# Kernel tuning notes

Hardware: AMD Instinct MI355X
Metric: run time of the kernel (lower is better)

The kernel has to match this reference:

```python
import jax, jax.numpy as jnp
import numpy as np

N_UNITS = 512
H = 8
D_K = N_UNITS // H  # 64
B = 4
T = 1024


def setup_inputs() -> dict:
    key = jax.random.key(0)
    ks = jax.random.split(key, 10)
    s = 0.02
    return {
        "x": jax.random.normal(ks[0], (B * T, N_UNITS), dtype=jnp.float32),
        "pos_k": jax.random.normal(ks[1], (T, T, D_K), dtype=jnp.float32),
        "batch_size": B,
        "Wq": jax.random.normal(ks[2], (N_UNITS, N_UNITS), dtype=jnp.float32) * s,
        "bq": jax.random.normal(ks[3], (N_UNITS,), dtype=jnp.float32) * s,
        "Wk": jax.random.normal(ks[4], (N_UNITS, N_UNITS), dtype=jnp.float32) * s,
        "bk": jax.random.normal(ks[5], (N_UNITS,), dtype=jnp.float32) * s,
        "Wv": jax.random.normal(ks[6], (N_UNITS, N_UNITS), dtype=jnp.float32) * s,
        "bv": jax.random.normal(ks[7], (N_UNITS,), dtype=jnp.float32) * s,
        "Wo": jax.random.normal(ks[8], (N_UNITS, N_UNITS), dtype=jnp.float32) * s,
        "bo": jax.random.normal(ks[9], (N_UNITS,), dtype=jnp.float32) * s,
    }


def reference(x, pos_k, batch_size, Wq, bq, Wk, bk, Wv, bv, Wo, bo):
    # x: [B*T, n_units]; pos_k: [T, T, d_k]
    q = (x @ Wq + bq).reshape(batch_size, -1, H, D_K).transpose(0, 2, 1, 3)  # [B,h,T,d]
    k = (x @ Wk + bk).reshape(batch_size, -1, H, D_K).transpose(0, 2, 1, 3)
    v = (x @ Wv + bv).reshape(batch_size, -1, H, D_K).transpose(0, 2, 1, 3)
    att_score = jnp.einsum("bhqd,bhkd->bhqk", q, k)
    # relative-position score: per query position t, q[:,:,t] @ pos_k[t].T
    att_score_pos = jnp.einsum("bhqd,qkd->bhqk", q, pos_k)
    scores = (att_score + att_score_pos) / np.sqrt(D_K).astype(np.float32)
    att = jax.nn.softmax(scores, axis=3)  # dropout p=0 -> identity (eval)
    out = jnp.einsum("bhqk,bhkd->bhqd", att, v)  # [B,h,T,d]
    out = out.transpose(0, 2, 1, 3).reshape(-1, H * D_K)  # [B*T, n_units]
    return out @ Wo + bo
```

## Files before the change

### kernel.cpp

```cpp
#include <hip/hip_runtime.h>


#define TT 1024
#define DH 64
#define NH 8
#define NBH 32
#define NU 512
#define NROW 4096

typedef __bf16 bf16;
typedef bf16 bf16x8 __attribute__((ext_vector_type(8)));
typedef bf16 bf16x4 __attribute__((ext_vector_type(4)));
typedef float f32x4 __attribute__((ext_vector_type(4)));

#define MFMA16(a, b, c) __builtin_amdgcn_mfma_f32_16x16x32_bf16(a, b, c, 0, 0, 0)

__global__ __launch_bounds__(256) void cvtx_k(const float* __restrict__ x,
                                              bf16* __restrict__ xb) {
  int i = blockIdx.x * 256 + threadIdx.x;
  float4 v = ((const float4*)x)[i];
  bf16x4 o = {(bf16)v.x, (bf16)v.y, (bf16)v.z, (bf16)v.w};
  ((bf16x4*)xb)[i] = o;
}

__global__ __launch_bounds__(256) void wtrans_k(const float* __restrict__ Wq,
                                                const float* __restrict__ Wk,
                                                const float* __restrict__ Wv,
                                                const float* __restrict__ Wo,
                                                bf16* __restrict__ wt) {
  int n = blockIdx.x * 256 + threadIdx.x;
  int k0 = blockIdx.y * 64;
  int w = blockIdx.z;
  const float* W = (w == 0) ? Wq : (w == 1) ? Wk : (w == 2) ? Wv : Wo;
  bf16* o = wt + ((size_t)w * NU + n) * NU;
  for (int kk = 0; kk < 64; kk += 8) {
    bf16x8 v;
#pragma unroll
    for (int j = 0; j < 8; j++) v[j] = (bf16)W[(size_t)(k0 + kk + j) * NU + n];
    *(bf16x8*)(o + k0 + kk) = v;
  }
}

__global__ __launch_bounds__(256) void qkv_k(
    const bf16* __restrict__ xb, const bf16* __restrict__ wt,
    const float* __restrict__ bq, const float* __restrict__ bk,
    const float* __restrict__ bv, bf16* __restrict__ Qb, bf16* __restrict__ Kb,
    bf16* __restrict__ Vt) {
  int tid = threadIdx.x, wid = tid >> 6, ln = tid & 63;
  int n15 = ln & 15, qd = ln >> 4;
  int n0 = blockIdx.x * 64, m0 = blockIdx.y * 64;
  int mrow = m0 + wid * 16 + n15;

  const f32x4 fz = {0.f, 0.f, 0.f, 0.f};
  f32x4 acc[3][4];
#pragma unroll
  for (int w = 0; w < 3; w++)
#pragma unroll
    for (int nt = 0; nt < 4; nt++) acc[w][nt] = fz;

  for (int k0 = 0; k0 < NU; k0 += 32) {
    bf16x8 a = *(const bf16x8*)(xb + (size_t)mrow * NU + k0 + qd * 8);
#pragma unroll
    for (int w = 0; w < 3; w++)
#pragma unroll
      for (int nt = 0; nt < 4; nt++) {
        bf16x8 b = *(const bf16x8*)(wt + ((size_t)w * NU + n0 + nt * 16 + n15) * NU +
                                    k0 + qd * 8);
        acc[w][nt] = MFMA16(a, b, acc[w][nt]);
      }
  }

  int bb = m0 >> 10;
  int tbase = (m0 & 1023) + wid * 16 + qd * 4;
  int hh = n0 >> 6;
#pragma unroll
  for (int nt = 0; nt < 4; nt++) {
    int d = nt * 16 + n15;
    float bqv = bq[n0 + d], bkv = bk[n0 + d], bvv = bv[n0 + d];
    bf16x4 vv;
#pragma unroll
    for (int r = 0; r < 4; r++) {
      int t = tbase + r;
      size_t qk_idx = ((size_t)(bb * NH + hh) * TT + t) * DH + d;
      Qb[qk_idx] = (bf16)(acc[0][nt][r] + bqv);
      Kb[qk_idx] = (bf16)(acc[1][nt][r] + bkv);
      vv[r] = (bf16)(acc[2][nt][r] + bvv);
    }
    *(bf16x4*)(Vt + ((size_t)(bb * NH + hh) * DH + d) * TT + tbase) = vv;
  }
}

__global__ __launch_bounds__(256) void pos_gemm_k(const float* __restrict__ pos,
                                                  const bf16* __restrict__ Qb,
                                                  bf16* __restrict__ biasS) {
  int tid = threadIdx.x, wid = tid >> 6, ln = tid & 63;
  int n15 = ln & 15, qd = ln >> 4;
  int t = blockIdx.y, s0 = blockIdx.x * 64;
  int mt = (wid & 1) * 16;
  int nb = (wid >> 1) * 2;

  bf16x8 aQ[2];
#pragma unroll
  for (int kc = 0; kc < 2; kc++)
    aQ[kc] = *(const bf16x8*)(Qb + ((size_t)(mt + n15) * TT + t) * DH + kc * 32 + qd * 8);

  const f32x4 fz = {0.f, 0.f, 0.f, 0.f};
  f32x4 acc[2] = {fz, fz};
#pragma unroll
  for (int ntl = 0; ntl < 2; ntl++) {
    int s = s0 + (nb + ntl) * 16 + n15;
    const float* pr = pos + ((size_t)t * TT + s) * DH + qd * 8;
#pragma unroll
    for (int kc = 0; kc < 2; kc++) {
      float4 u = *(const float4*)(pr + kc * 32);
      float4 v = *(const float4*)(pr + kc * 32 + 4);
      bf16x8 bfr = {(bf16)u.x, (bf16)u.y, (bf16)u.z, (bf16)u.w,
                    (bf16)v.x, (bf16)v.y, (bf16)v.z, (bf16)v.w};
      acc[ntl] = MFMA16(aQ[kc], bfr, acc[ntl]);
    }
  }
#pragma unroll
  for (int ntl = 0; ntl < 2; ntl++)
#pragma unroll
    for (int r = 0; r < 4; r++) {
      int s = s0 + (nb + ntl) * 16 + n15;
      int bhh = mt + qd * 4 + r;
      biasS[((size_t)bhh * TT + t) * TT + s] = (bf16)acc[ntl][r];
    }
}

__global__ __launch_bounds__(256) void flash_k(const bf16* __restrict__ Qb,
                                               const bf16* __restrict__ Kb,
                                               const bf16* __restrict__ Vt,
                                               const bf16* __restrict__ biasS,
                                               bf16* __restrict__ att) {
  int tid = threadIdx.x, wid = tid >> 6, ln = tid & 63;
  int n15 = ln & 15, qd = ln >> 4;
  int bh = blockIdx.x;
  int t0 = blockIdx.y * 64 + wid * 16;
  const float SC = 0.18033688f;

  __shared__ bf16 Pl[4][16][40];

  bf16x8 aQ[2];
#pragma unroll
  for (int kc = 0; kc < 2; kc++)
    aQ[kc] = *(const bf16x8*)(Qb + ((size_t)bh * TT + t0 + n15) * DH + kc * 32 + qd * 8);

  const f32x4 fz = {0.f, 0.f, 0.f, 0.f};
  f32x4 accO[4] = {fz, fz, fz, fz};
  f32x4 accL = fz;
  const bf16 one = (bf16)1.0f;
  const bf16x8 onesv = {one, one, one, one, one, one, one, one};

  const size_t brow = (size_t)bh * TT;
  float bvs[2][4];
#pragma unroll
  for (int ntl = 0; ntl < 2; ntl++)
#pragma unroll
    for (int r = 0; r < 4; r++)
      bvs[ntl][r] = (float)biasS[(brow + t0 + qd * 4 + r) * TT + ntl * 16 + n15];

  for (int s0 = 0; s0 < TT; s0 += 32) {
    int sp = (s0 + 32) & 1023;
    float bnx[2][4];
#pragma unroll
    for (int ntl = 0; ntl < 2; ntl++)
#pragma unroll
      for (int r = 0; r < 4; r++)
        bnx[ntl][r] = (float)biasS[(brow + t0 + qd * 4 + r) * TT + sp + ntl * 16 + n15];

    f32x4 accS[2] = {fz, fz};
#pragma unroll
    for (int ntl = 0; ntl < 2; ntl++)
#pragma unroll
      for (int kc = 0; kc < 2; kc++) {
        bf16x8 bK = *(const bf16x8*)(Kb + ((size_t)bh * TT + s0 + ntl * 16 + n15) * DH +
                                     kc * 32 + qd * 8);
        accS[ntl] = MFMA16(aQ[kc], bK, accS[ntl]);
      }

#pragma unroll
    for (int ntl = 0; ntl < 2; ntl++)
#pragma unroll
      for (int r = 0; r < 4; r++) {
        float p = __builtin_amdgcn_exp2f((accS[ntl][r] + bvs[ntl][r]) * SC);
        Pl[wid][qd * 4 + r][ntl * 16 + n15] = (bf16)p;
      }
#pragma unroll
    for (int ntl = 0; ntl < 2; ntl++)
#pragma unroll
      for (int r = 0; r < 4; r++) bvs[ntl][r] = bnx[ntl][r];

    bf16x8 aP = *(const bf16x8*)(&Pl[wid][n15][qd * 8]);
    accL = MFMA16(aP, onesv, accL);
#pragma unroll
    for (int dt = 0; dt < 4; dt++) {
      bf16x8 bV = *(const bf16x8*)(Vt + ((size_t)bh * DH + dt * 16 + n15) * TT + s0 + qd * 8);
      accO[dt] = MFMA16(aP, bV, accO[dt]);
    }
  }

  int bb = bh >> 3, hh = bh & 7;
#pragma unroll
  for (int dt = 0; dt < 4; dt++)
#pragma unroll
    for (int r = 0; r < 4; r++) {
      int t = t0 + qd * 4 + r;
      float o = accO[dt][r] / accL[r];
      att[((size_t)bb * TT + t) * NU + hh * DH + dt * 16 + n15] = (bf16)o;
    }
}

__global__ __launch_bounds__(256) void proj_k(const bf16* __restrict__ att,
                                              const bf16* __restrict__ wt,
                                              const float* __restrict__ bo,
                                              float* __restrict__ out) {
  int tid = threadIdx.x, wid = tid >> 6, ln = tid & 63;
  int n15 = ln & 15, qd = ln >> 4;
  int n0 = blockIdx.x * 64, m0 = blockIdx.y * 64;
  int mrow = m0 + wid * 16 + n15;

  const f32x4 fz = {0.f, 0.f, 0.f, 0.f};
  f32x4 acc[4] = {fz, fz, fz, fz};
  for (int k0 = 0; k0 < NU; k0 += 32) {
    bf16x8 a = *(const bf16x8*)(att + (size_t)mrow * NU + k0 + qd * 8);
#pragma unroll
    for (int nt = 0; nt < 4; nt++) {
      bf16x8 b = *(const bf16x8*)(wt + ((size_t)3 * NU + n0 + nt * 16 + n15) * NU +
                                  k0 + qd * 8);
      acc[nt] = MFMA16(a, b, acc[nt]);
    }
  }
#pragma unroll
  for (int nt = 0; nt < 4; nt++) {
    int col = n0 + nt * 16 + n15;
    float bov = bo[col];
#pragma unroll
    for (int r = 0; r < 4; r++) {
      int row = m0 + wid * 16 + qd * 4 + r;
      out[(size_t)row * NU + col] = acc[nt][r] + bov;
    }
  }
}

extern "C" void kernel_launch(void* const* d_in, const int* in_sizes, int n_in,
                              void* d_out, int out_size, void* d_ws, size_t ws_size,
                              hipStream_t stream) {
  const float* x = (const float*)d_in[0];
  const float* pos = (const float*)d_in[1];
  const float* Wq = (const float*)d_in[3];
  const float* bq = (const float*)d_in[4];
  const float* Wk = (const float*)d_in[5];
  const float* bk = (const float*)d_in[6];
  const float* Wv = (const float*)d_in[7];
  const float* bv = (const float*)d_in[8];
  const float* Wo = (const float*)d_in[9];
  const float* bo = (const float*)d_in[10];
  float* out = (float*)d_out;

  char* ws = (char*)d_ws;
  bf16* xb = (bf16*)(ws);
  bf16* wt = (bf16*)(ws + ((size_t)4 << 20));
  bf16* Qb = (bf16*)(ws + ((size_t)6 << 20));
  bf16* Kb = (bf16*)(ws + ((size_t)10 << 20));
  bf16* Vt = (bf16*)(ws + ((size_t)14 << 20));
  bf16* att = (bf16*)(ws + ((size_t)18 << 20));
  bf16* biasS = (bf16*)(ws + ((size_t)22 << 20));

  cvtx_k<<<2048, 256, 0, stream>>>(x, xb);
  wtrans_k<<<dim3(2, 8, 4), 256, 0, stream>>>(Wq, Wk, Wv, Wo, wt);
  qkv_k<<<dim3(8, 64), 256, 0, stream>>>(xb, wt, bq, bk, bv, Qb, Kb, Vt);
  pos_gemm_k<<<dim3(16, 1024), 256, 0, stream>>>(pos, Qb, biasS);
  flash_k<<<dim3(32, 16), 256, 0, stream>>>(Qb, Kb, Vt, biasS, att);
  proj_k<<<dim3(8, 64), 256, 0, stream>>>(att, wt, bo, out);
}
```

Baseline: 562.2 us.

## Restructure pos GEMM, pipeline flash loads, transpose MFMA operands, widen wtrans grid

The pos_gemm kernel now stages the 32 query rows for each t in shared memory, and each wave covers all 32 bh rows over a 128-wide s tile. It reads pos_k with nontemporal loads, so the dominant fp32 pos stream is read once per element with fewer blocks. The flash kernel swaps its MFMA operand order (K·Q and V·P) so scores and the bias load come out contiguous per lane. It also double-buffers K/V fragments and runs bias loads two steps ahead in registers, and writes the output vectorised. The weight-transpose kernel launches 8x more blocks with one 8-element chunk each, for more parallelism. Register pressure in flash rises from the prefetch buffers.

```diff
diff --git a/kernel.cpp b/kernel.cpp
--- a/kernel.cpp
+++ b/kernel.cpp
@@ -4,9 +4,7 @@
 #define TT 1024
 #define DH 64
 #define NH 8
-#define NBH 32
 #define NU 512
-#define NROW 4096
 
 typedef __bf16 bf16;
 typedef bf16 bf16x8 __attribute__((ext_vector_type(8)));
@@ -29,16 +27,13 @@
                                                 const float* __restrict__ Wo,
                                                 bf16* __restrict__ wt) {
   int n = blockIdx.x * 256 + threadIdx.x;
-  int k0 = blockIdx.y * 64;
+  int k0 = blockIdx.y * 8;
   int w = blockIdx.z;
   const float* W = (w == 0) ? Wq : (w == 1) ? Wk : (w == 2) ? Wv : Wo;
-  bf16* o = wt + ((size_t)w * NU + n) * NU;
-  for (int kk = 0; kk < 64; kk += 8) {
-    bf16x8 v;
-#pragma unroll
-    for (int j = 0; j < 8; j++) v[j] = (bf16)W[(size_t)(k0 + kk + j) * NU + n];
-    *(bf16x8*)(o + k0 + kk) = v;
-  }
+  bf16x8 v;
+#pragma unroll
+  for (int j = 0; j < 8; j++) v[j] = (bf16)W[(size_t)(k0 + j) * NU + n];
+  *(bf16x8*)(wt + ((size_t)w * NU + n) * NU + k0) = v;
 }
 
 __global__ __launch_bounds__(256) void qkv_k(
@@ -95,38 +90,55 @@
                                                   bf16* __restrict__ biasS) {
   int tid = threadIdx.x, wid = tid >> 6, ln = tid & 63;
   int n15 = ln & 15, qd = ln >> 4;
-  int t = blockIdx.y, s0 = blockIdx.x * 64;
-  int mt = (wid & 1) * 16;
-  int nb = (wid >> 1) * 2;
-
-  bf16x8 aQ[2];
-#pragma unroll
-  for (int kc = 0; kc < 2; kc++)
-    aQ[kc] = *(const bf16x8*)(Qb + ((size_t)(mt + n15) * TT + t) * DH + kc * 32 + qd * 8);
-
-  const f32x4 fz = {0.f, 0.f, 0.f, 0.f};
-  f32x4 acc[2] = {fz, fz};
+  int t = blockIdx.y;
+  int s0b = blockIdx.x * 128;
+
+  __shared__ bf16 Qs[32 * 72];
+  {
+    int bh = tid >> 3, dc = (tid & 7) * 8;
+    bf16x8 q = *(const bf16x8*)(Qb + ((size_t)bh * TT + t) * DH + dc);
+    *(bf16x8*)(&Qs[bh * 72 + dc]) = q;
+  }
+  __syncthreads();
+
+  bf16x8 aQ[2][2];
+#pragma unroll
+  for (int mt = 0; mt < 2; mt++)
+#pragma unroll
+    for (int kc = 0; kc < 2; kc++)
+      aQ[mt][kc] = *(const bf16x8*)(&Qs[(mt * 16 + n15) * 72 + kc * 32 + qd * 8]);
+
+  const f32x4 fz = {0.f, 0.f, 0.f, 0.f};
+  f32x4 acc[2][2];
+#pragma unroll
+  for (int mt = 0; mt < 2; mt++)
+#pragma unroll
+    for (int ntl = 0; ntl < 2; ntl++) acc[mt][ntl] = fz;
+
 #pragma unroll
   for (int ntl = 0; ntl < 2; ntl++) {
-    int s = s0 + (nb + ntl) * 16 + n15;
+    int s = s0b + (wid * 2 + ntl) * 16 + n15;
     const float* pr = pos + ((size_t)t * TT + s) * DH + qd * 8;
 #pragma unroll
     for (int kc = 0; kc < 2; kc++) {
-      float4 u = *(const float4*)(pr + kc * 32);
-      float4 v = *(const float4*)(pr + kc * 32 + 4);
-      bf16x8 bfr = {(bf16)u.x, (bf16)u.y, (bf16)u.z, (bf16)u.w,
-                    (bf16)v.x, (bf16)v.y, (bf16)v.z, (bf16)v.w};
-      acc[ntl] = MFMA16(aQ[kc], bfr, acc[ntl]);
-    }
-  }
-#pragma unroll
-  for (int ntl = 0; ntl < 2; ntl++)
-#pragma unroll
-    for (int r = 0; r < 4; r++) {
-      int s = s0 + (nb + ntl) * 16 + n15;
-      int bhh = mt + qd * 4 + r;
-      biasS[((size_t)bhh * TT + t) * TT + s] = (bf16)acc[ntl][r];
-    }
+      f32x4 u = __builtin_nontemporal_load((const f32x4*)(pr + kc * 32));
+      f32x4 v = __builtin_nontemporal_load((const f32x4*)(pr + kc * 32 + 4));
+      bf16x8 bB = {(bf16)u[0], (bf16)u[1], (bf16)u[2], (bf16)u[3],
+                   (bf16)v[0], (bf16)v[1], (bf16)v[2], (bf16)v[3]};
+#pragma unroll
+      for (int mt = 0; mt < 2; mt++) acc[mt][ntl] = MFMA16(aQ[mt][kc], bB, acc[mt][ntl]);
+    }
+  }
+#pragma unroll
+  for (int mt = 0; mt < 2; mt++)
+#pragma unroll
+    for (int ntl = 0; ntl < 2; ntl++)
+#pragma unroll
+      for (int r = 0; r < 4; r++) {
+        int s = s0b + (wid * 2 + ntl) * 16 + n15;
+        int bh = mt * 16 + qd * 4 + r;
+        biasS[((size_t)bh * TT + t) * TT + s] = (bf16)acc[mt][ntl][r];
+      }
 }
 
 __global__ __launch_bounds__(256) void flash_k(const bf16* __restrict__ Qb,
@@ -142,10 +154,14 @@
 
   __shared__ bf16 Pl[4][16][40];
 
-  bf16x8 aQ[2];
+  bf16x8 bQ[2];
 #pragma unroll
   for (int kc = 0; kc < 2; kc++)
-    aQ[kc] = *(const bf16x8*)(Qb + ((size_t)bh * TT + t0 + n15) * DH + kc * 32 + qd * 8);
+    bQ[kc] = *(const bf16x8*)(Qb + ((size_t)bh * TT + t0 + n15) * DH + kc * 32 + qd * 8);
+
+  const bf16* Kbase = Kb + (size_t)bh * TT * DH;
+  const bf16* Vbase = Vt + (size_t)bh * DH * TT;
+  const bf16* Bbase = biasS + ((size_t)bh * TT + t0 + n15) * TT;
 
   const f32x4 fz = {0.f, 0.f, 0.f, 0.f};
   f32x4 accO[4] = {fz, fz, fz, fz};
@@ -153,63 +169,68 @@
   const bf16 one = (bf16)1.0f;
   const bf16x8 onesv = {one, one, one, one, one, one, one, one};
 
-  const size_t brow = (size_t)bh * TT;
-  float bvs[2][4];
-#pragma unroll
-  for (int ntl = 0; ntl < 2; ntl++)
-#pragma unroll
-    for (int r = 0; r < 4; r++)
-      bvs[ntl][r] = (float)biasS[(brow + t0 + qd * 4 + r) * TT + ntl * 16 + n15];
-
-  for (int s0 = 0; s0 < TT; s0 += 32) {
-    int sp = (s0 + 32) & 1023;
-    float bnx[2][4];
-#pragma unroll
-    for (int ntl = 0; ntl < 2; ntl++)
-#pragma unroll
-      for (int r = 0; r < 4; r++)
-        bnx[ntl][r] = (float)biasS[(brow + t0 + qd * 4 + r) * TT + sp + ntl * 16 + n15];
+  bf16x8 Kf[2][4], Vf[2][4];
+  bf16x4 Bf[4][2];
+
+  auto ldKV = [&](int buf, int s0) {
+#pragma unroll
+    for (int mt = 0; mt < 2; mt++)
+#pragma unroll
+      for (int kc = 0; kc < 2; kc++)
+        Kf[buf][mt * 2 + kc] =
+            *(const bf16x8*)(Kbase + (size_t)(s0 + mt * 16 + n15) * DH + kc * 32 + qd * 8);
+#pragma unroll
+    for (int dt = 0; dt < 4; dt++)
+      Vf[buf][dt] = *(const bf16x8*)(Vbase + (size_t)(dt * 16 + n15) * TT + s0 + qd * 8);
+  };
+  auto ldB = [&](int buf, int s0) {
+#pragma unroll
+    for (int mt = 0; mt < 2; mt++)
+      Bf[buf][mt] = *(const bf16x4*)(Bbase + s0 + mt * 16 + qd * 4);
+  };
+
+  ldB(0, 0);
+  ldB(1, 32);
+  ldKV(0, 0);
+
+#pragma unroll 4
+  for (int it = 0; it < 32; it++) {
+    int s0 = it * 32;
+    ldKV((it + 1) & 1, (s0 + 32) & 1023);
+    ldB((it + 2) & 3, (s0 + 64) & 1023);
 
     f32x4 accS[2] = {fz, fz};
 #pragma unroll
-    for (int ntl = 0; ntl < 2; ntl++)
-#pragma unroll
-      for (int kc = 0; kc < 2; kc++) {
-        bf16x8 bK = *(const bf16x8*)(Kb + ((size_t)bh * TT + s0 + ntl * 16 + n15) * DH +
-                                     kc * 32 + qd * 8);
-        accS[ntl] = MFMA16(aQ[kc], bK, accS[ntl]);
+    for (int mt = 0; mt < 2; mt++)
+#pragma unroll
+      for (int kc = 0; kc < 2; kc++)
+        accS[mt] = MFMA16(Kf[it & 1][mt * 2 + kc], bQ[kc], accS[mt]);
+
+#pragma unroll
+    for (int mt = 0; mt < 2; mt++) {
+      bf16x4 pb;
+#pragma unroll
+      for (int r = 0; r < 4; r++) {
+        float p = __builtin_amdgcn_exp2f((accS[mt][r] + (float)Bf[it & 3][mt][r]) * SC);
+        pb[r] = (bf16)p;
       }
-
-#pragma unroll
-    for (int ntl = 0; ntl < 2; ntl++)
-#pragma unroll
-      for (int r = 0; r < 4; r++) {
-        float p = __builtin_amdgcn_exp2f((accS[ntl][r] + bvs[ntl][r]) * SC);
-        Pl[wid][qd * 4 + r][ntl * 16 + n15] = (bf16)p;
-      }
-#pragma unroll
-    for (int ntl = 0; ntl < 2; ntl++)
-#pragma unroll
-      for (int r = 0; r < 4; r++) bvs[ntl][r] = bnx[ntl][r];
-
-    bf16x8 aP = *(const bf16x8*)(&Pl[wid][n15][qd * 8]);
-    accL = MFMA16(aP, onesv, accL);
-#pragma unroll
-    for (int dt = 0; dt < 4; dt++) {
-      bf16x8 bV = *(const bf16x8*)(Vt + ((size_t)bh * DH + dt * 16 + n15) * TT + s0 + qd * 8);
-      accO[dt] = MFMA16(aP, bV, accO[dt]);
-    }
+      *(bf16x4*)(&Pl[wid][n15][mt * 16 + qd * 4]) = pb;
+    }
+    bf16x8 bP = *(const bf16x8*)(&Pl[wid][n15][qd * 8]);
+    accL = MFMA16(onesv, bP, accL);
+#pragma unroll
+    for (int dt = 0; dt < 4; dt++) accO[dt] = MFMA16(Vf[it & 1][dt], bP, accO[dt]);
   }
 
   int bb = bh >> 3, hh = bh & 7;
-#pragma unroll
-  for (int dt = 0; dt < 4; dt++)
-#pragma unroll
-    for (int r = 0; r < 4; r++) {
-      int t = t0 + qd * 4 + r;
-      float o = accO[dt][r] / accL[r];
-      att[((size_t)bb * TT + t) * NU + hh * DH + dt * 16 + n15] = (bf16)o;
-    }
+  float rcp = 1.0f / accL[0];
+#pragma unroll
+  for (int dt = 0; dt < 4; dt++) {
+    bf16x4 ov;
+#pragma unroll
+    for (int r = 0; r < 4; r++) ov[r] = (bf16)(accO[dt][r] * rcp);
+    *(bf16x4*)(att + ((size_t)bb * TT + t0 + n15) * NU + hh * DH + dt * 16 + qd * 4) = ov;
+  }
 }
 
 __global__ __launch_bounds__(256) void proj_k(const bf16* __restrict__ att,
@@ -269,9 +290,9 @@
   bf16* biasS = (bf16*)(ws + ((size_t)22 << 20));
 
   cvtx_k<<<2048, 256, 0, stream>>>(x, xb);
-  wtrans_k<<<dim3(2, 8, 4), 256, 0, stream>>>(Wq, Wk, Wv, Wo, wt);
+  wtrans_k<<<dim3(2, 64, 4), 256, 0, stream>>>(Wq, Wk, Wv, Wo, wt);
   qkv_k<<<dim3(8, 64), 256, 0, stream>>>(xb, wt, bq, bk, bv, Qb, Kb, Vt);
-  pos_gemm_k<<<dim3(16, 1024), 256, 0, stream>>>(pos, Qb, biasS);
+  pos_gemm_k<<<dim3(8, 1024), 256, 0, stream>>>(pos, Qb, biasS);
   flash_k<<<dim3(32, 16), 256, 0, stream>>>(Qb, Kb, Vt, biasS, att);
   proj_k<<<dim3(8, 64), 256, 0, stream>>>(att, wt, bo, out);
 }
```

New measurement: 538.2 us. 1.04x faster.
